# Optimization experiments

Measured on AMD Instinct MI355X. Metric: run time of the kernel, lower is better.

Reference implementation:

```python
import jax, jax.numpy as jnp
import numpy as np

B, H, W, C = 512, 7, 7, 768


def _conv3(v, k, b):
    # 1-channel conv1d, kernel size 3, padding 1. v: (B, L), k: (3,), b: scalar
    vp = jnp.pad(v, ((0, 0), (1, 1)))
    return k[0] * vp[:, :-2] + k[1] * vp[:, 1:-1] + k[2] * vp[:, 2:] + b


def setup_inputs() -> dict:
    key = jax.random.key(0)
    ks = jax.random.split(key, 32)
    n = lambda i, shape, s=0.02: jax.random.normal(ks[i], shape, dtype=jnp.float32) * s
    inp = {
        "x": jax.random.normal(ks[0], (B, H, W, C), dtype=jnp.float32),
        # 1x1 Conv2d(dim,dim) weights stored as (out,in)
        "Wh": n(1, (C, C)), "bh": n(2, (C,)),
        "Ww": n(3, (C, C)), "bw": n(4, (C,)),
        "Ws": n(5, (C, C)), "bs": n(6, (C,)),
        # Conv1d(1,1,1) -> scalar weight/bias
        "convH_w": n(7, ()), "convH_b": n(8, ()),
        "convH2_k": n(9, (3,)), "convH2_b": n(10, ()),
        # Conv1d(2,1,1)
        "mixhw_k": n(11, (2,)), "mixhw_b": n(12, ()),
        "mixhw2_k": n(13, (3,)), "mixhw2_b": n(14, ()),
        # Conv1d(3,1,1)
        "mixhws_k": n(15, (3,)), "mixhws_b": n(16, ()),
        "mixhws2_k": n(17, (3,)), "mixhws2_b": n(18, ()),
        # Linear(7, dim)
        "linH_W": n(19, (C, 7), 0.1), "linH_b": n(20, (C,)),
        "linW_W": n(21, (C, 7), 0.1), "linW_b": n(22, (C,)),
        # mix_all: Conv2d(3*dim, dim, 1)
        "mixall_W": n(23, (C, 3 * C)), "mixall_b": n(24, (C,)),
        # proj: Linear(dim, dim)
        "proj_W": n(25, (C, C)), "proj_b": n(26, (C,)),
        "gate_weights": jnp.ones((2,), dtype=jnp.float32),
    }
    return inp


def reference(x, Wh, bh, Ww, bw, Ws, bs, convH_w, convH_b, convH2_k, convH2_b,
              mixhw_k, mixhw_b, mixhw2_k, mixhw2_b, mixhws_k, mixhws_b,
              mixhws2_k, mixhws2_b, linH_W, linH_b, linW_W, linW_b,
              mixall_W, mixall_b, proj_W, proj_b, gate_weights):
    gelu = lambda v: jax.nn.gelu(v, approximate=False)
    sig = jax.nn.sigmoid
    add = x

    # H branch: mlp_h (1x1 conv over channels), pool over (W, C) per H index
    h = gelu(jnp.einsum('bhwc,dc->bhwd', x, Wh) + bh)          # (B,H,W,C)
    h2v = h.mean(axis=(2, 3))                                   # (B,H)
    g_h = sig(_conv3(sig(h2v * convH_w + convH_b), convH2_k, convH2_b))  # (B,H)
    h3 = h * g_h[:, :, None, None]                              # gate per H index

    # W branch: pool over (H, C) per W index, gate mixed with H stats
    w = gelu(jnp.einsum('bhwc,dc->bhwd', x, Ww) + bw)           # (B,H,W,C)
    w2v = w.mean(axis=(1, 3))                                   # (B,W)
    g_hw = sig(_conv3(sig(mixhw_k[0] * h2v + mixhw_k[1] * w2v + mixhw_b),
                      mixhw2_k, mixhw2_b))                      # (B,W)
    w3 = w * g_hw[:, None, :, None]                             # gate per W index

    # C branch: pool over (H, W) per channel, gate mixed with lifted H/W stats
    s = gelu(jnp.einsum('bhwc,dc->bhwd', x, Ws) + bs)           # (B,H,W,C)
    s1v = s.mean(axis=(1, 2))                                   # (B,C)
    h2l = h2v @ linH_W.T + linH_b                               # (B,C)
    w2l = w2v @ linW_W.T + linW_b                               # (B,C)
    g_c = sig(_conv3(sig(mixhws_k[0] * h2l + mixhws_k[1] * w2l
                         + mixhws_k[2] * s1v + mixhws_b),
                     mixhws2_k, mixhws2_b))                     # (B,C)
    s2 = s * g_c[:, None, None, :]                              # gate per channel

    # concat along channel dim + 1x1 mixing conv + proj
    cat = jnp.concatenate([h3, w3, s2], axis=-1)                # (B,H,W,3C)
    mixed = jnp.einsum('bhwk,dk->bhwd', cat, mixall_W) + mixall_b
    out = mixed @ proj_W.T + proj_b
    out = out * gate_weights[0] + add * gate_weights[1]
    return out
```

## Files before the change

### kernel.cpp

```cpp
#include <hip/hip_runtime.h>
#include <cstdint>
#include <cstddef>

typedef __attribute__((ext_vector_type(8))) __bf16 bf16x8;
typedef __attribute__((ext_vector_type(4))) float f32x4;

__device__ __forceinline__ float sigm(float v) { return 1.0f / (1.0f + expf(-v)); }

__device__ __forceinline__ float gelu_fast(float v) {
  float u = v * (1.0f + 0.044715f * v * v);
  float z = 1.5957691216057308f * u;
  return v / (1.0f + __expf(-z));
}

__device__ __forceinline__ void async16(__bf16* lds, const __bf16* g) {
  __builtin_amdgcn_global_load_lds(
      (const __attribute__((address_space(1))) void*)g,
      (__attribute__((address_space(3))) void*)lds, 16, 0, 0);
}

__global__ __launch_bounds__(256) void k_convert(const float* __restrict__ src,
                                                 __bf16* __restrict__ dst, int n8) {
  int i = blockIdx.x * 256 + threadIdx.x;
  if (i >= n8) return;
  const f32x4* s4 = (const f32x4*)src;
  f32x4 a = s4[2 * i], b = s4[2 * i + 1];
  bf16x8 o;
#pragma unroll
  for (int e = 0; e < 4; ++e) { o[e] = (__bf16)a[e]; o[4 + e] = (__bf16)b[e]; }
  ((bf16x8*)dst)[i] = o;
}

__global__ __launch_bounds__(256) void k_prep(
    const float* __restrict__ Wh, const float* __restrict__ Ww,
    const float* __restrict__ Ws, const float* __restrict__ projW,
    const float* __restrict__ bh, const float* __restrict__ bw,
    const float* __restrict__ bs, const float* __restrict__ mixallb,
    const float* __restrict__ projb, __bf16* __restrict__ Wcat,
    __bf16* __restrict__ Pb, float* __restrict__ bcat, float* __restrict__ b2) {
  const int bid = blockIdx.x, t = threadIdx.x;
  if (bid < 1152) {
    const int seg = bid / 288, loc = bid % 288;
    const float* src = seg == 0 ? Wh : (seg == 1 ? Ww : (seg == 2 ? Ws : projW));
    __bf16* dst = seg == 3 ? Pb : Wcat + (size_t)seg * 589824;
    const int i = loc * 256 + t;
    const f32x4* s4 = (const f32x4*)src;
    f32x4 a = s4[2 * i], b = s4[2 * i + 1];
    bf16x8 o;
#pragma unroll
    for (int e = 0; e < 4; ++e) { o[e] = (__bf16)a[e]; o[4 + e] = (__bf16)b[e]; }
    ((bf16x8*)dst)[i] = o;
  } else if (bid < 1161) {
    const int i = (bid - 1152) * 256 + t;
    if (i < 2304)
      bcat[i] = i < 768 ? bh[i] : (i < 1536 ? bw[i - 768] : bs[i - 1536]);
  } else {
    const int d = (bid - 1161) * 256 + t;
    float acc = projb[d];
    const float* row = projW + (size_t)d * 768;
#pragma unroll 4
    for (int c = 0; c < 768; c += 4) {
      f32x4 p4 = *(const f32x4*)(row + c);
      f32x4 b4 = *(const f32x4*)(mixallb + c);
      acc += p4[0] * b4[0] + p4[1] * b4[1] + p4[2] * b4[2] + p4[3] * b4[3];
    }
    b2[d] = acc;
  }
}

__global__ __launch_bounds__(256) void k_transpose_cvt(const float* __restrict__ src,
                                                       __bf16* __restrict__ dst,
                                                       int R, int C) {
  __shared__ float t[32][33];
  const int c0 = blockIdx.x * 32, r0 = blockIdx.y * 32;
  const int tx = threadIdx.x, ty = threadIdx.y;
#pragma unroll
  for (int i = 0; i < 32; i += 8)
    if (r0 + ty + i < R && c0 + tx < C) t[ty + i][tx] = src[(size_t)(r0 + ty + i) * C + c0 + tx];
  __syncthreads();
#pragma unroll
  for (int i = 0; i < 32; i += 8)
    if (c0 + ty + i < C && r0 + tx < R)
      dst[(size_t)(c0 + ty + i) * R + r0 + tx] = (__bf16)t[tx][ty + i];
}

template <int EPI>
__device__ __forceinline__ void gemm_body(
    __bf16* lds, const __bf16* __restrict__ A, const __bf16* __restrict__ B,
    const float* __restrict__ bias, __bf16* __restrict__ outB,
    float* __restrict__ outF, const float* __restrict__ xres,
    const float* __restrict__ gatew, int N, int K, int tm, int tn) {
  const int tid = threadIdx.x;
  const int lane = tid & 63, wid = tid >> 6;
  const int wr = wid >> 1, wc = wid & 1;

  const __bf16* Ag = A + (size_t)tm * 256 * K;
  const __bf16* Bg = B + (size_t)tn * 128 * K;

  auto stage = [&](int buf, int kt) {
    const int base = buf * 12288;
#pragma unroll
    for (int j = 0; j < 4; ++j) {
      const int lin = j * 256 + tid;
      const int row = lin >> 2, ch = lin & 3;
      async16(&lds[base + lin * 8],
              Ag + (size_t)row * K + kt * 32 + ((ch ^ ((row >> 1) & 3)) << 3));
    }
#pragma unroll
    for (int j = 0; j < 2; ++j) {
      const int lin = j * 256 + tid;
      const int row = lin >> 2, ch = lin & 3;
      async16(&lds[base + 8192 + lin * 8],
              Bg + (size_t)row * K + kt * 32 + ((ch ^ ((row >> 1) & 3)) << 3));
    }
  };

  f32x4 acc[8][4];
#pragma unroll
  for (int m = 0; m < 8; ++m)
#pragma unroll
    for (int n = 0; n < 4; ++n) acc[m][n] = f32x4{0.f, 0.f, 0.f, 0.f};

  const int kc = lane >> 4;
  const int rA = wr * 128 + (lane & 15);
  const int rB = wc * 64 + (lane & 15);
  const int chA = kc ^ ((rA >> 1) & 3);
  const int chB = kc ^ ((rB >> 1) & 3);
  const int NT = K >> 5;

  stage(0, 0);
  stage(1, 1);
  asm volatile("s_waitcnt vmcnt(6)" ::: "memory");
  __builtin_amdgcn_s_barrier();

  for (int t = 0; t < NT; ++t) {
    const int cb = (t % 3) * 12288;
    if (t + 2 < NT) stage((t + 2) % 3, t + 2);
    bf16x8 af[8], bfv[4];
#pragma unroll
    for (int m = 0; m < 8; ++m)
      af[m] = *(const bf16x8*)&lds[cb + (rA + m * 16) * 32 + chA * 8];
#pragma unroll
    for (int n = 0; n < 4; ++n)
      bfv[n] = *(const bf16x8*)&lds[cb + 8192 + (rB + n * 16) * 32 + chB * 8];
    __builtin_amdgcn_s_setprio(1);
#pragma unroll
    for (int m = 0; m < 8; ++m)
#pragma unroll
      for (int n = 0; n < 4; ++n)
        acc[m][n] = __builtin_amdgcn_mfma_f32_16x16x32_bf16(af[m], bfv[n], acc[m][n], 0, 0, 0);
    __builtin_amdgcn_s_setprio(0);
    if (t + 2 < NT) { asm volatile("s_waitcnt vmcnt(6)" ::: "memory"); }
    else            { asm volatile("s_waitcnt vmcnt(0)" ::: "memory"); }
    __builtin_amdgcn_s_barrier();
  }

  const int orow = (lane >> 4) * 4;
  const int ocol = lane & 15;
  float g0 = 0.f, g1 = 0.f;
  if constexpr (EPI == 2) { g0 = gatew[0]; g1 = gatew[1]; }
#pragma unroll
  for (int m = 0; m < 8; ++m) {
#pragma unroll
    for (int n = 0; n < 4; ++n) {
#pragma unroll
      for (int rr = 0; rr < 4; ++rr) {
        const int rg = tm * 256 + wr * 128 + m * 16 + orow + rr;
        const int cg = tn * 128 + wc * 64 + n * 16 + ocol;
        if constexpr (EPI == 0) {
          float v = acc[m][n][rr] + bias[cg];
          outB[(size_t)rg * N + cg] = (__bf16)gelu_fast(v);
        } else if constexpr (EPI == 2) {
          float v = acc[m][n][rr] + bias[cg];
          outF[(size_t)rg * N + cg] = g0 * v + g1 * xres[(size_t)rg * N + cg];
        } else {
          outB[(size_t)rg * N + cg] = (__bf16)acc[m][n][rr];
        }
      }
    }
  }
}

__device__ __forceinline__ int swz_bij(int b, int nwg) {
  const int q = nwg >> 3, r = nwg & 7;
  const int xcd = b & 7, idx = b >> 3;
  return (xcd < r ? xcd * (q + 1) : r * (q + 1) + (xcd - r) * q) + idx;
}

__global__ __launch_bounds__(256, 2) void k_gemm_fused(
    const __bf16* __restrict__ Pb, const __bf16* __restrict__ Dt,
    __bf16* __restrict__ W2, const __bf16* __restrict__ xb,
    const __bf16* __restrict__ Wcat, const float* __restrict__ bcat,
    __bf16* __restrict__ hws) {
  __shared__ __bf16 lds[36864];
  if (blockIdx.x < 54) {
    const int tm = blockIdx.x / 18, tn = blockIdx.x % 18;
    gemm_body<3>(lds, Pb, Dt, nullptr, W2, nullptr, nullptr, nullptr,
                 2304, 768, tm, tn);
  } else {
    const int wgid = swz_bij(blockIdx.x - 54, 1764);
    gemm_body<0>(lds, xb, Wcat, bcat, hws, nullptr, nullptr, nullptr,
                 2304, 768, wgid / 18, wgid % 18);
  }
}

__global__ __launch_bounds__(256, 2) void k_gemm2(
    const __bf16* __restrict__ hws, const __bf16* __restrict__ W2,
    const float* __restrict__ b2, float* __restrict__ out,
    const float* __restrict__ x, const float* __restrict__ gatew) {
  __shared__ __bf16 lds[36864];
  const int wgid = swz_bij(blockIdx.x, 588);
  gemm_body<2>(lds, hws, W2, b2, nullptr, out, x, gatew,
               768, 2304, wgid / 6, wgid % 6);
}

__global__ __launch_bounds__(256) void k_poolgate(
    __bf16* __restrict__ hws, const float* __restrict__ convH_w,
    const float* __restrict__ convH_b, const float* __restrict__ convH2_k,
    const float* __restrict__ convH2_b, const float* __restrict__ mixhw_k,
    const float* __restrict__ mixhw_b, const float* __restrict__ mixhw2_k,
    const float* __restrict__ mixhw2_b, const float* __restrict__ mixhws_k,
    const float* __restrict__ mixhws_b, const float* __restrict__ mixhws2_k,
    const float* __restrict__ mixhws2_b, const float* __restrict__ linHW,
    const float* __restrict__ linHb, const float* __restrict__ linWW,
    const float* __restrict__ linWb) {
  const int b = blockIdx.x, t = threadIdx.x;
  const int lane = t & 63, wave = t >> 6;
  const size_t base = (size_t)b * 49 * 2304;

  __shared__ float red[4][14];
  __shared__ float s1v[768];
  __shared__ float hv[7], wv[7];
  __shared__ float ghl[7], ghwl[7];
  __shared__ float tc[770];
  __shared__ float gcl[768];

  float hloc[7], wloc[7];
#pragma unroll
  for (int i = 0; i < 7; ++i) { hloc[i] = 0.f; wloc[i] = 0.f; }
  float sacc[8], sacc2[8];
#pragma unroll
  for (int e = 0; e < 8; ++e) { sacc[e] = 0.f; sacc2[e] = 0.f; }

  const bool isH = t < 96, isW = (t >= 96 && t < 192);
  const int off1 = isH ? t * 8 : (isW ? 768 + (t - 96) * 8 : 1536 + (t - 192) * 8);
  const int off2 = 1536 + (64 + t) * 8;

#pragma unroll
  for (int p = 0; p < 49; ++p) {
    const int hi = p / 7, wi = p % 7;
    const __bf16* row = hws + base + (size_t)p * 2304;
    bf16x8 v = *(const bf16x8*)(row + off1);
    float s8 = 0.f;
#pragma unroll
    for (int e = 0; e < 8; ++e) s8 += (float)v[e];
    if (isH) hloc[hi] += s8;
    else if (isW) wloc[wi] += s8;
    else {
#pragma unroll
      for (int e = 0; e < 8; ++e) sacc[e] += (float)v[e];
    }
    if (t < 32) {
      bf16x8 v2 = *(const bf16x8*)(row + off2);
#pragma unroll
      for (int e = 0; e < 8; ++e) sacc2[e] += (float)v2[e];
    }
  }

  if (t >= 192) {
#pragma unroll
    for (int e = 0; e < 8; ++e) s1v[(t - 192) * 8 + e] = sacc[e] * (1.f / 49.f);
  }
  if (t < 32) {
#pragma unroll
    for (int e = 0; e < 8; ++e) s1v[512 + t * 8 + e] = sacc2[e] * (1.f / 49.f);
  }

#pragma unroll
  for (int i = 0; i < 7; ++i) {
    float hvx = hloc[i], wvx = wloc[i];
#pragma unroll
    for (int s = 32; s; s >>= 1) { hvx += __shfl_xor(hvx, s); wvx += __shfl_xor(wvx, s); }
    if (lane == 0) { red[wave][i] = hvx; red[wave][7 + i] = wvx; }
  }
  if (t == 8) { tc[0] = 0.f; tc[769] = 0.f; }
  __syncthreads();

  if (t < 7) {
    hv[t] = (red[0][t] + red[1][t] + red[2][t] + red[3][t]) * (1.f / 5376.f);
  } else if (t >= 16 && t < 23) {
    const int i = t - 16;
    wv[i] = (red[0][7 + i] + red[1][7 + i] + red[2][7 + i] + red[3][7 + i]) * (1.f / 5376.f);
  }
  __syncthreads();

  if (t < 7) {
    const float cw = convH_w[0], cbv = convH_b[0];
    const float k0 = convH2_k[0], k1 = convH2_k[1], k2 = convH2_k[2], b2v = convH2_b[0];
    const float um = t > 0 ? sigm(hv[t - 1] * cw + cbv) : 0.f;
    const float u0 = sigm(hv[t] * cw + cbv);
    const float up = t < 6 ? sigm(hv[t + 1] * cw + cbv) : 0.f;
    ghl[t] = sigm(k0 * um + k1 * u0 + k2 * up + b2v);

    const float a0 = mixhw_k[0], a1 = mixhw_k[1], ab = mixhw_b[0];
    const float q0 = mixhw2_k[0], q1 = mixhw2_k[1], q2 = mixhw2_k[2], qb = mixhw2_b[0];
    const float vm = t > 0 ? sigm(a0 * hv[t - 1] + a1 * wv[t - 1] + ab) : 0.f;
    const float v0 = sigm(a0 * hv[t] + a1 * wv[t] + ab);
    const float vp = t < 6 ? sigm(a0 * hv[t + 1] + a1 * wv[t + 1] + ab) : 0.f;
    ghwl[t] = sigm(q0 * vm + q1 * v0 + q2 * vp + qb);
  }

  const float m0 = mixhws_k[0], m1 = mixhws_k[1], m2 = mixhws_k[2], mb = mixhws_b[0];
#pragma unroll
  for (int j = 0; j < 3; ++j) {
    const int c = t + j * 256;
    float h2l = linHb[c], w2l = linWb[c];
#pragma unroll
    for (int i = 0; i < 7; ++i) {
      h2l += hv[i] * linHW[c * 7 + i];
      w2l += wv[i] * linWW[c * 7 + i];
    }
    tc[1 + c] = sigm(m0 * h2l + m1 * w2l + m2 * s1v[c] + mb);
  }
  __syncthreads();
  const float r0 = mixhws2_k[0], r1 = mixhws2_k[1], r2 = mixhws2_k[2], rb2 = mixhws2_b[0];
#pragma unroll
  for (int j = 0; j < 3; ++j) {
    const int c = t + j * 256;
    gcl[c] = sigm(r0 * tc[c] + r1 * tc[c + 1] + r2 * tc[c + 2] + rb2);
  }
  __syncthreads();

  bf16x8* slab = (bf16x8*)(hws + base);
  for (int i = t; i < 49 * 288; i += 256) {
    const int k8 = i % 288, p = i / 288;
    bf16x8 v = slab[i];
    if (k8 < 96) {
      const float g = ghl[p / 7];
#pragma unroll
      for (int e = 0; e < 8; ++e) v[e] = (__bf16)((float)v[e] * g);
    } else if (k8 < 192) {
      const float g = ghwl[p % 7];
#pragma unroll
      for (int e = 0; e < 8; ++e) v[e] = (__bf16)((float)v[e] * g);
    } else {
      const float* gcp = gcl + (k8 - 192) * 8;
#pragma unroll
      for (int e = 0; e < 8; ++e) v[e] = (__bf16)((float)v[e] * gcp[e]);
    }
    slab[i] = v;
  }
}

extern "C" void kernel_launch(void* const* d_in, const int* in_sizes, int n_in,
                              void* d_out, int out_size, void* d_ws, size_t ws_size,
                              hipStream_t stream) {
  const float* x        = (const float*)d_in[0];
  const float* Wh       = (const float*)d_in[1];
  const float* bh       = (const float*)d_in[2];
  const float* Ww       = (const float*)d_in[3];
  const float* bw       = (const float*)d_in[4];
  const float* Ws       = (const float*)d_in[5];
  const float* bs       = (const float*)d_in[6];
  const float* convH_w  = (const float*)d_in[7];
  const float* convH_b  = (const float*)d_in[8];
  const float* convH2_k = (const float*)d_in[9];
  const float* convH2_b = (const float*)d_in[10];
  const float* mixhw_k  = (const float*)d_in[11];
  const float* mixhw_b  = (const float*)d_in[12];
  const float* mixhw2_k = (const float*)d_in[13];
  const float* mixhw2_b = (const float*)d_in[14];
  const float* mixhws_k = (const float*)d_in[15];
  const float* mixhws_b = (const float*)d_in[16];
  const float* mixhws2_k= (const float*)d_in[17];
  const float* mixhws2_b= (const float*)d_in[18];
  const float* linHW    = (const float*)d_in[19];
  const float* linHb    = (const float*)d_in[20];
  const float* linWW    = (const float*)d_in[21];
  const float* linWb    = (const float*)d_in[22];
  const float* mixallW  = (const float*)d_in[23];
  const float* mixallb  = (const float*)d_in[24];
  const float* projW    = (const float*)d_in[25];
  const float* projb    = (const float*)d_in[26];
  const float* gatew    = (const float*)d_in[27];
  float* out = (float*)d_out;
  (void)in_sizes; (void)n_in; (void)out_size; (void)ws_size;

  const int M = 25088;
  char* ws = (char*)d_ws;
  size_t off = 0;
  auto carve = [&](size_t bytes) -> void* {
    void* p = ws + off;
    off += (bytes + 255) & ~(size_t)255;
    return p;
  };
  __bf16* xb     = (__bf16*)carve((size_t)M * 768 * 2);
  __bf16* Wcat   = (__bf16*)carve((size_t)2304 * 768 * 2);
  __bf16* Pb     = (__bf16*)carve((size_t)768 * 768 * 2);
  __bf16* Dt     = (__bf16*)carve((size_t)2304 * 768 * 2);
  __bf16* W2     = (__bf16*)carve((size_t)768 * 2304 * 2);
  float*  bcat   = (float*)carve(2304 * 4);
  float*  b2     = (float*)carve(768 * 4);
  __bf16* hws    = (__bf16*)carve((size_t)M * 2304 * 2);

  k_convert<<<9408, 256, 0, stream>>>(x, xb, (M * 768) / 8);
  k_prep<<<1164, 256, 0, stream>>>(Wh, Ww, Ws, projW, bh, bw, bs, mixallb, projb,
                                   Wcat, Pb, bcat, b2);
  k_transpose_cvt<<<dim3(72, 24), dim3(32, 8), 0, stream>>>(mixallW, Dt, 768, 2304);

  k_gemm_fused<<<54 + 1764, 256, 0, stream>>>(Pb, Dt, W2, xb, Wcat, bcat, hws);
  k_poolgate<<<512, 256, 0, stream>>>(hws, convH_w, convH_b, convH2_k, convH2_b,
                                      mixhw_k, mixhw_b, mixhw2_k, mixhw2_b,
                                      mixhws_k, mixhws_b, mixhws2_k, mixhws2_b,
                                      linHW, linHb, linWW, linWb);
  k_gemm2<<<98 * 6, 256, 0, stream>>>(hws, W2, b2, out, x, gatew);
}
```

Measured before the change: 375.1 us.

## Split-K the tail tiles of final GEMM and merge prep kernels

Merges the input conversion, weight prep and mixall transpose into a single launch to cut launch overhead. For the final GEMM, the last 78 output tiles are split into two K halves computed by separate workgroups, with partial results combined by a new reduction kernel. This is meant to reduce tail-wave imbalance, at the cost of an extra scratch buffer, an extra launch, and extra memory traffic.

Measured after the change: 368.7 us, median of 2. No clear change (-1.7%).

```diff
diff --git a/kernel.cpp b/kernel.cpp
--- a/kernel.cpp
+++ b/kernel.cpp
@@ -19,69 +19,66 @@
       (__attribute__((address_space(3))) void*)lds, 16, 0, 0);
 }
 
-__global__ __launch_bounds__(256) void k_convert(const float* __restrict__ src,
-                                                 __bf16* __restrict__ dst, int n8) {
-  int i = blockIdx.x * 256 + threadIdx.x;
-  if (i >= n8) return;
-  const f32x4* s4 = (const f32x4*)src;
-  f32x4 a = s4[2 * i], b = s4[2 * i + 1];
-  bf16x8 o;
-#pragma unroll
-  for (int e = 0; e < 4; ++e) { o[e] = (__bf16)a[e]; o[4 + e] = (__bf16)b[e]; }
-  ((bf16x8*)dst)[i] = o;
-}
-
-__global__ __launch_bounds__(256) void k_prep(
+__global__ __launch_bounds__(256) void k_prep_all(
+    const float* __restrict__ x, __bf16* __restrict__ xb,
     const float* __restrict__ Wh, const float* __restrict__ Ww,
     const float* __restrict__ Ws, const float* __restrict__ projW,
     const float* __restrict__ bh, const float* __restrict__ bw,
     const float* __restrict__ bs, const float* __restrict__ mixallb,
     const float* __restrict__ projb, __bf16* __restrict__ Wcat,
-    __bf16* __restrict__ Pb, float* __restrict__ bcat, float* __restrict__ b2) {
+    __bf16* __restrict__ Pb, float* __restrict__ bcat, float* __restrict__ b2,
+    const float* __restrict__ mixallW, __bf16* __restrict__ Dt) {
+  __shared__ float tsh[32][33];
   const int bid = blockIdx.x, t = threadIdx.x;
-  if (bid < 1152) {
-    const int seg = bid / 288, loc = bid % 288;
-    const float* src = seg == 0 ? Wh : (seg == 1 ? Ww : (seg == 2 ? Ws : projW));
-    __bf16* dst = seg == 3 ? Pb : Wcat + (size_t)seg * 589824;
-    const int i = loc * 256 + t;
-    const f32x4* s4 = (const f32x4*)src;
+  if (bid < 9408) {
+    const int i = bid * 256 + t;
+    const f32x4* s4 = (const f32x4*)x;
     f32x4 a = s4[2 * i], b = s4[2 * i + 1];
     bf16x8 o;
 #pragma unroll
     for (int e = 0; e < 4; ++e) { o[e] = (__bf16)a[e]; o[4 + e] = (__bf16)b[e]; }
-    ((bf16x8*)dst)[i] = o;
-  } else if (bid < 1161) {
-    const int i = (bid - 1152) * 256 + t;
-    if (i < 2304)
-      bcat[i] = i < 768 ? bh[i] : (i < 1536 ? bw[i - 768] : bs[i - 1536]);
+    ((bf16x8*)xb)[i] = o;
+  } else if (bid < 10572) {
+    const int pb_ = bid - 9408;
+    if (pb_ < 1152) {
+      const int seg = pb_ / 288, loc = pb_ % 288;
+      const float* src = seg == 0 ? Wh : (seg == 1 ? Ww : (seg == 2 ? Ws : projW));
+      __bf16* dst = seg == 3 ? Pb : Wcat + (size_t)seg * 589824;
+      const int i = loc * 256 + t;
+      const f32x4* s4 = (const f32x4*)src;
+      f32x4 a = s4[2 * i], b = s4[2 * i + 1];
+      bf16x8 o;
+#pragma unroll
+      for (int e = 0; e < 4; ++e) { o[e] = (__bf16)a[e]; o[4 + e] = (__bf16)b[e]; }
+      ((bf16x8*)dst)[i] = o;
+    } else if (pb_ < 1161) {
+      const int i = (pb_ - 1152) * 256 + t;
+      if (i < 2304)
+        bcat[i] = i < 768 ? bh[i] : (i < 1536 ? bw[i - 768] : bs[i - 1536]);
+    } else {
+      const int d = (pb_ - 1161) * 256 + t;
+      float acc = projb[d];
+      const float* row = projW + (size_t)d * 768;
+#pragma unroll 4
+      for (int c = 0; c < 768; c += 4) {
+        f32x4 p4 = *(const f32x4*)(row + c);
+        f32x4 b4 = *(const f32x4*)(mixallb + c);
+        acc += p4[0] * b4[0] + p4[1] * b4[1] + p4[2] * b4[2] + p4[3] * b4[3];
+      }
+      b2[d] = acc;
+    }
   } else {
-    const int d = (bid - 1161) * 256 + t;
-    float acc = projb[d];
-    const float* row = projW + (size_t)d * 768;
-#pragma unroll 4
-    for (int c = 0; c < 768; c += 4) {
-      f32x4 p4 = *(const f32x4*)(row + c);
-      f32x4 b4 = *(const f32x4*)(mixallb + c);
-      acc += p4[0] * b4[0] + p4[1] * b4[1] + p4[2] * b4[2] + p4[3] * b4[3];
-    }
-    b2[d] = acc;
-  }
-}
-
-__global__ __launch_bounds__(256) void k_transpose_cvt(const float* __restrict__ src,
-                                                       __bf16* __restrict__ dst,
-                                                       int R, int C) {
-  __shared__ float t[32][33];
-  const int c0 = blockIdx.x * 32, r0 = blockIdx.y * 32;
-  const int tx = threadIdx.x, ty = threadIdx.y;
-#pragma unroll
-  for (int i = 0; i < 32; i += 8)
-    if (r0 + ty + i < R && c0 + tx < C) t[ty + i][tx] = src[(size_t)(r0 + ty + i) * C + c0 + tx];
-  __syncthreads();
-#pragma unroll
-  for (int i = 0; i < 32; i += 8)
-    if (c0 + ty + i < C && r0 + tx < R)
-      dst[(size_t)(c0 + ty + i) * R + r0 + tx] = (__bf16)t[tx][ty + i];
+    const int lb = bid - 10572;
+    const int c0 = (lb % 72) * 32, r0 = (lb / 72) * 32;
+    const int tx = t & 31, ty = t >> 5;
+#pragma unroll
+    for (int i = 0; i < 32; i += 8)
+      tsh[ty + i][tx] = mixallW[(size_t)(r0 + ty + i) * 2304 + c0 + tx];
+    __syncthreads();
+#pragma unroll
+    for (int i = 0; i < 32; i += 8)
+      Dt[(size_t)(c0 + ty + i) * 768 + r0 + tx] = (__bf16)tsh[tx][ty + i];
+  }
 }
 
 template <int EPI>
@@ -89,13 +86,14 @@
     __bf16* lds, const __bf16* __restrict__ A, const __bf16* __restrict__ B,
     const float* __restrict__ bias, __bf16* __restrict__ outB,
     float* __restrict__ outF, const float* __restrict__ xres,
-    const float* __restrict__ gatew, int N, int K, int tm, int tn) {
+    const float* __restrict__ gatew, int N, int Kstride, int Klen, int koff,
+    int tm, int tn) {
   const int tid = threadIdx.x;
   const int lane = tid & 63, wid = tid >> 6;
   const int wr = wid >> 1, wc = wid & 1;
 
-  const __bf16* Ag = A + (size_t)tm * 256 * K;
-  const __bf16* Bg = B + (size_t)tn * 128 * K;
+  const __bf16* Ag = A + (size_t)tm * 256 * Kstride + koff;
+  const __bf16* Bg = B + (size_t)tn * 128 * Kstride + koff;
 
   auto stage = [&](int buf, int kt) {
     const int base = buf * 12288;
@@ -104,14 +102,14 @@
       const int lin = j * 256 + tid;
       const int row = lin >> 2, ch = lin & 3;
       async16(&lds[base + lin * 8],
-              Ag + (size_t)row * K + kt * 32 + ((ch ^ ((row >> 1) & 3)) << 3));
+              Ag + (size_t)row * Kstride + kt * 32 + ((ch ^ ((row >> 1) & 3)) << 3));
     }
 #pragma unroll
     for (int j = 0; j < 2; ++j) {
       const int lin = j * 256 + tid;
       const int row = lin >> 2, ch = lin & 3;
       async16(&lds[base + 8192 + lin * 8],
-              Bg + (size_t)row * K + kt * 32 + ((ch ^ ((row >> 1) & 3)) << 3));
+              Bg + (size_t)row * Kstride + kt * 32 + ((ch ^ ((row >> 1) & 3)) << 3));
     }
   };
 
@@ -126,7 +124,7 @@
   const int rB = wc * 64 + (lane & 15);
   const int chA = kc ^ ((rA >> 1) & 3);
   const int chB = kc ^ ((rB >> 1) & 3);
-  const int NT = K >> 5;
+  const int NT = Klen >> 5;
 
   stage(0, 0);
   stage(1, 1);
@@ -158,7 +156,7 @@
   const int orow = (lane >> 4) * 4;
   const int ocol = lane & 15;
   float g0 = 0.f, g1 = 0.f;
-  if constexpr (EPI == 2) { g0 = gatew[0]; g1 = gatew[1]; }
+  if constexpr (EPI == 2 || EPI == 5 || EPI == 6) { g0 = gatew[0]; g1 = gatew[1]; }
 #pragma unroll
   for (int m = 0; m < 8; ++m) {
 #pragma unroll
@@ -170,9 +168,11 @@
         if constexpr (EPI == 0) {
           float v = acc[m][n][rr] + bias[cg];
           outB[(size_t)rg * N + cg] = (__bf16)gelu_fast(v);
-        } else if constexpr (EPI == 2) {
+        } else if constexpr (EPI == 2 || EPI == 5) {
           float v = acc[m][n][rr] + bias[cg];
           outF[(size_t)rg * N + cg] = g0 * v + g1 * xres[(size_t)rg * N + cg];
+        } else if constexpr (EPI == 6) {
+          outF[(size_t)(rg - 21760) * 768 + cg] = g0 * acc[m][n][rr];
         } else {
           outB[(size_t)rg * N + cg] = (__bf16)acc[m][n][rr];
         }
@@ -196,22 +196,46 @@
   if (blockIdx.x < 54) {
     const int tm = blockIdx.x / 18, tn = blockIdx.x % 18;
     gemm_body<3>(lds, Pb, Dt, nullptr, W2, nullptr, nullptr, nullptr,
-                 2304, 768, tm, tn);
+                 2304, 768, 768, 0, tm, tn);
   } else {
     const int wgid = swz_bij(blockIdx.x - 54, 1764);
     gemm_body<0>(lds, xb, Wcat, bcat, hws, nullptr, nullptr, nullptr,
-                 2304, 768, wgid / 18, wgid % 18);
+                 2304, 768, 768, 0, wgid / 18, wgid % 18);
   }
 }
 
 __global__ __launch_bounds__(256, 2) void k_gemm2(
     const __bf16* __restrict__ hws, const __bf16* __restrict__ W2,
     const float* __restrict__ b2, float* __restrict__ out,
-    const float* __restrict__ x, const float* __restrict__ gatew) {
+    const float* __restrict__ x, const float* __restrict__ gatew,
+    float* __restrict__ pT) {
   __shared__ __bf16 lds[36864];
-  const int wgid = swz_bij(blockIdx.x, 588);
-  gemm_body<2>(lds, hws, W2, b2, nullptr, out, x, gatew,
-               768, 2304, wgid / 6, wgid % 6);
+  const int bid = blockIdx.x;
+  if (bid < 510) {
+    const int wgid = swz_bij(bid, 510);
+    gemm_body<2>(lds, hws, W2, b2, nullptr, out, x, gatew,
+                 768, 2304, 2304, 0, wgid / 6, wgid % 6);
+  } else if (bid < 588) {
+    const int i = bid - 510;
+    gemm_body<5>(lds, hws, W2, b2, nullptr, out, x, gatew,
+                 768, 2304, 1152, 0, 85 + i / 6, i % 6);
+  } else {
+    const int i = bid - 588;
+    gemm_body<6>(lds, hws, W2, b2, nullptr, pT, x, gatew,
+                 768, 2304, 1152, 1152, 85 + i / 6, i % 6);
+  }
+}
+
+__global__ __launch_bounds__(256) void k_tailred(float* __restrict__ out,
+                                                 const float* __restrict__ pT) {
+  const int i = blockIdx.x * 256 + threadIdx.x;
+  if (i >= 638976) return;
+  f32x4* o = (f32x4*)(out + (size_t)21760 * 768);
+  f32x4 a = o[i];
+  f32x4 b = ((const f32x4*)pT)[i];
+#pragma unroll
+  for (int e = 0; e < 4; ++e) a[e] += b[e];
+  o[i] = a;
 }
 
 __global__ __launch_bounds__(256) void k_poolgate(
@@ -402,16 +426,16 @@
   float*  bcat   = (float*)carve(2304 * 4);
   float*  b2     = (float*)carve(768 * 4);
   __bf16* hws    = (__bf16*)carve((size_t)M * 2304 * 2);
-
-  k_convert<<<9408, 256, 0, stream>>>(x, xb, (M * 768) / 8);
-  k_prep<<<1164, 256, 0, stream>>>(Wh, Ww, Ws, projW, bh, bw, bs, mixallb, projb,
-                                   Wcat, Pb, bcat, b2);
-  k_transpose_cvt<<<dim3(72, 24), dim3(32, 8), 0, stream>>>(mixallW, Dt, 768, 2304);
-
+  float*  pT     = (float*)carve((size_t)3328 * 768 * 4);
+
+  k_prep_all<<<12300, 256, 0, stream>>>(x, xb, Wh, Ww, Ws, projW, bh, bw, bs,
+                                        mixallb, projb, Wcat, Pb, bcat, b2,
+                                        mixallW, Dt);
   k_gemm_fused<<<54 + 1764, 256, 0, stream>>>(Pb, Dt, W2, xb, Wcat, bcat, hws);
   k_poolgate<<<512, 256, 0, stream>>>(hws, convH_w, convH_b, convH2_k, convH2_b,
                                       mixhw_k, mixhw_b, mixhw2_k, mixhw2_b,
                                       mixhws_k, mixhws_b, mixhws2_k, mixhws2_b,
                                       linHW, linHb, linWW, linWb);
-  k_gemm2<<<98 * 6, 256, 0, stream>>>(hws, W2, b2, out, x, gatew);
-}
+  k_gemm2<<<666, 256, 0, stream>>>(hws, W2, b2, out, x, gatew, pT);
+  k_tailred<<<2496, 256, 0, stream>>>(out, pT);
+}
```
